# Kernel optimization log

Measured on AMD Instinct MI355X. Metric: run time of the kernel, lower is better.

The kernel has to match this reference:

```python
import jax, jax.numpy as jnp
import numpy as np

N = 8192      # nodes
E = 16384     # edges
G = 512       # graphs
IN = 235      # node feature dim (input_dim)
H = 64        # hidden_dim
ED = 52       # edge feature dim


def setup_inputs() -> dict:
    key = jax.random.key(0)
    ks = jax.random.split(key, 24)
    s = lambda fan_in: 1.0 / np.sqrt(fan_in)
    inp = {}
    inp["x"] = jax.random.normal(ks[0], (N, IN), dtype=jnp.float32)
    inp["edge_index"] = jax.random.randint(ks[1], (2, E), 0, N)
    inp["edge_attr"] = jax.random.uniform(ks[2], (E, ED), dtype=jnp.float32)
    inp["batch"] = jnp.sort(jax.random.randint(ks[3], (N,), 0, G))
    # EdgeModel (nn of nnconv1): Linear(52,128) -> Linear(128, 235*64)
    inp["W1"] = jax.random.normal(ks[4], (128, ED), dtype=jnp.float32) * s(ED)
    inp["b1"] = jnp.zeros((128,), jnp.float32)
    inp["W2"] = jax.random.normal(ks[5], (IN * H, 128), dtype=jnp.float32) * s(128)
    inp["b2"] = jnp.zeros((IN * H,), jnp.float32)
    # NNConv root weight and bias
    inp["root"] = jax.random.normal(ks[6], (IN, H), dtype=jnp.float32) * s(IN)
    inp["conv_b"] = jnp.zeros((H,), jnp.float32)
    # MLP head
    inp["fw1"] = jax.random.normal(ks[7], (128, H), dtype=jnp.float32) * s(H)
    inp["fb1"] = jnp.zeros((128,), jnp.float32)
    inp["fw2"] = jax.random.normal(ks[8], (256, 128), dtype=jnp.float32) * s(128)
    inp["fb2"] = jnp.zeros((256,), jnp.float32)
    inp["fw3"] = jax.random.normal(ks[9], (128, 256), dtype=jnp.float32) * s(256)
    inp["fb3"] = jnp.zeros((128,), jnp.float32)
    inp["fw4"] = jax.random.normal(ks[10], (1, 128), dtype=jnp.float32) * s(128)
    inp["fb4"] = jnp.zeros((1,), jnp.float32)
    return inp


def reference(x, edge_index, edge_attr, batch, W1, b1, W2, b2, root, conv_b,
              fw1, fb1, fw2, fb2, fw3, fb3, fw4, fb4):
    src, dst = edge_index[0], edge_index[1]
    # edge MLP -> per-edge weight matrices [E, IN, H]
    h = edge_attr @ W1.T + b1
    w = (h @ W2.T + b2).reshape(E, IN, H)
    # gather source node feats, per-edge matmul, scatter-add to destinations
    msg = jnp.einsum('ei,eih->eh', x[src], w)          # [E, H]
    agg = jax.ops.segment_sum(msg, dst, num_segments=N)  # [N, H]
    out = jax.nn.relu(agg + x @ root + conv_b)           # NNConv + ReLU
    # global mean pool per graph
    summ = jax.ops.segment_sum(out, batch, num_segments=G)
    cnt = jax.ops.segment_sum(jnp.ones((N, 1), out.dtype), batch, num_segments=G)
    pooled = summ / jnp.maximum(cnt, 1.0)                # [G, H]
    # dense MLP head
    y = jax.nn.relu(pooled @ fw1.T + fb1)
    y = jax.nn.relu(y @ fw2.T + fb2)
    y = jax.nn.relu(y @ fw3.T + fb3)
    return y @ fw4.T + fb4                               # [G, 1]
```

## Files before the change

### kernel.cpp

```cpp
#include <hip/hip_runtime.h>
#include <hip/hip_bf16.h>
#include <stdint.h>

#define N_NODES 8192
#define N_EDGES 16384
#define N_GRAPHS 512
#define IN_DIM 235
#define H_DIM 64
#define ED_DIM 52
#define HID1 128
#define KP 256
#define NB 3328
#define NBP 3584


#define BT_BLOCKS 940
#define EXT_BLOCKS 128
#define ZERO_BLOCKS 16
#define A_BLOCKS 1024
#define PREP_GRID (BT_BLOCKS + EXT_BLOCKS + ZERO_BLOCKS + A_BLOCKS)

#define GEMM_GRID 1728

typedef __bf16 bf16x8 __attribute__((ext_vector_type(8)));
typedef float f32x4 __attribute__((ext_vector_type(4)));

static __device__ inline unsigned short f2bf(float f) {
    union { float f; unsigned u; } v; v.f = f;
    unsigned r = v.u + 0x7FFFu + ((v.u >> 16) & 1u);
    return (unsigned short)(r >> 16);
}

__global__ __launch_bounds__(256) void k_prep(const float* __restrict__ x,
                                              const float* __restrict__ W1,
                                              const float* __restrict__ W2,
                                              const float* __restrict__ b1,
                                              const float* __restrict__ b2,
                                              const float* __restrict__ root,
                                              unsigned short* __restrict__ A,
                                              unsigned short* __restrict__ Bt) {
    __shared__ float w1s[ED_DIM * 132];
    __shared__ float w2s[16 * 132];
    const int bx = blockIdx.x;
    const int t = threadIdx.x;

    if (bx < BT_BLOCKS) {
        const int i = bx >> 2;
        const int by = bx & 3;
        for (int j = t; j < ED_DIM * HID1; j += 256) {
            const int k = j / ED_DIM, d = j - k * ED_DIM;
            w1s[d * 132 + k] = W1[j];
        }
        const float* w2src = W2 + ((size_t)i * 64 + by * 16) * HID1;
        for (int j = t; j < 16 * HID1; j += 256) w2s[(j >> 7) * 132 + (j & 127)] = w2src[j];
        __syncthreads();
        const int hh = t & 15, dq = t >> 4;
        const int h = by * 16 + hh;
        const float4* w2v = (const float4*)&w2s[hh * 132];
        #pragma unroll
        for (int m = 0; m < 4; ++m) {
            const int d = dq + m * 16;
            if (d >= ED_DIM) break;
            const float4* w1v = (const float4*)&w1s[d * 132];
            float acc = 0.f;
            #pragma unroll
            for (int k4 = 0; k4 < HID1 / 4; ++k4) {
                const float4 a = w1v[k4], b = w2v[k4];
                acc += a.x * b.x + a.y * b.y + a.z * b.z + a.w * b.w;
            }
            const int p = ((d >> 2) << 8) + h * 4 + (d & 3);
            Bt[(size_t)p * KP + i] = f2bf(acc);
        }
    } else if (bx < BT_BLOCKS + EXT_BLOCKS) {
        const int j = bx - BT_BLOCKS;
        const int i = t;
        if (i < IN_DIM) {
            float v;
            if (j < 64) {
                v = root[i * H_DIM + j];
            } else {
                const int jj = i * H_DIM + (j - 64);
                float acc = b2[jj];
                const float4* w = (const float4*)(W2 + (size_t)jj * HID1);
                const float4* bv = (const float4*)b1;
                #pragma unroll
                for (int k4 = 0; k4 < HID1 / 4; ++k4) {
                    const float4 a = w[k4], b = bv[k4];
                    acc += a.x * b.x; acc += a.y * b.y; acc += a.z * b.z; acc += a.w * b.w;
                }
                v = acc;
            }
            Bt[(size_t)(NB + j) * KP + i] = f2bf(v);
        }
    } else if (bx < BT_BLOCKS + EXT_BLOCKS + ZERO_BLOCKS) {
        const int z = bx - BT_BLOCKS - EXT_BLOCKS;
        const int TOT = 3456 * 21;
        for (int idx = z * 256 + t; idx < TOT; idx += ZERO_BLOCKS * 256) {
            const int r = idx / 21, c = IN_DIM + idx - r * 21;
            Bt[(size_t)r * KP + c] = 0;
        }
    } else {
        const int j8 = (bx - BT_BLOCKS - EXT_BLOCKS - ZERO_BLOCKS) * 256 + t;
        const int n = j8 >> 5, i0 = (j8 & 31) * 8;
        const float* xr = x + (size_t)n * IN_DIM;
        union { unsigned short us[8]; uint4 q; } pk;
        #pragma unroll
        for (int k = 0; k < 8; ++k) {
            const int i = i0 + k;
            pk.us[k] = (i < IN_DIM) ? f2bf(xr[i]) : (unsigned short)0;
        }
        *(uint4*)(&A[(size_t)j8 * 8]) = pk.q;
    }
}

__global__ __launch_bounds__(256) void k_gemm(const unsigned short* __restrict__ A,
                                              const unsigned short* __restrict__ Bt,
                                              unsigned short* __restrict__ P,
                                              float* __restrict__ agg,
                                              float* __restrict__ xb2,
                                              const float* __restrict__ conv_b) {
    __shared__ unsigned short As[2 * 128 * 32];
    __shared__ unsigned short Bs[2 * 128 * 32];
    const int t = threadIdx.x;
    const int lin = blockIdx.x;
    const int xcd = lin & 7, bi = lin >> 3;
    const int mt = (bi / 27) * 8 + xcd;
    const int nt = bi % 27;
    const int m0 = mt * 128, n0 = nt * 128;
    const int wid = t >> 6, lane = t & 63;
    const int wm = wid & 1;
    const int wn = wid >> 1;
    const int q = lane >> 4, r16 = lane & 15;

    f32x4 acc[4][4] = {};

    auto stage = [&](int k0, int buf) {
        #pragma unroll
        for (int s = 0; s < 2; ++s) {
            const int idx = s * 256 + t;
            const int row = idx >> 2;
            const int lgrp = ((idx & 3) ^ ((row >> 1) & 3)) * 8;
            const unsigned short* ga = &A[(size_t)(m0 + row) * KP + k0 + lgrp];
            const unsigned short* gb = &Bt[(size_t)(n0 + row) * KP + k0 + lgrp];
            char* la = (char*)As + buf * 8192 + s * 4096 + wid * 1024;
            char* lb = (char*)Bs + buf * 8192 + s * 4096 + wid * 1024;
            __builtin_amdgcn_global_load_lds(
                (const __attribute__((address_space(1))) unsigned int*)ga,
                (__attribute__((address_space(3))) unsigned int*)la, 16, 0, 0);
            __builtin_amdgcn_global_load_lds(
                (const __attribute__((address_space(1))) unsigned int*)gb,
                (__attribute__((address_space(3))) unsigned int*)lb, 16, 0, 0);
        }
    };

    stage(0, 0);
    const int pcq = (q ^ ((r16 >> 1) & 3)) * 8;
    #pragma unroll
    for (int it = 0; it < 8; ++it) {
        __syncthreads();
        if (it < 7) stage((it + 1) * 32, (it + 1) & 1);
        const int bo = (it & 1) * 4096;
        bf16x8 af[4], bfr[4];
        #pragma unroll
        for (int mi = 0; mi < 4; ++mi)
            af[mi] = *(const bf16x8*)(&As[bo + (wm * 64 + mi * 16 + r16) * 32 + pcq]);
        #pragma unroll
        for (int ni = 0; ni < 4; ++ni)
            bfr[ni] = *(const bf16x8*)(&Bs[bo + (wn * 64 + ni * 16 + r16) * 32 + pcq]);
        #pragma unroll
        for (int mi = 0; mi < 4; ++mi)
            #pragma unroll
            for (int ni = 0; ni < 4; ++ni)
                acc[mi][ni] = __builtin_amdgcn_mfma_f32_16x16x32_bf16(
                    bfr[ni], af[mi], acc[mi][ni], 0, 0, 0);
    }

    if (nt < 26) {
        #pragma unroll
        for (int mi = 0; mi < 4; ++mi)
            #pragma unroll
            for (int ni = 0; ni < 4; ++ni) {
                const int row = m0 + wm * 64 + mi * 16 + r16;
                const int col = n0 + wn * 64 + ni * 16 + q * 4;
                union { unsigned short us[4]; uint2 u2; } pk;
                #pragma unroll
                for (int rr = 0; rr < 4; ++rr) pk.us[rr] = f2bf(acc[mi][ni][rr]);
                *(uint2*)(&P[(size_t)row * NB + col]) = pk.u2;
            }
    } else {
        #pragma unroll
        for (int mi = 0; mi < 4; ++mi)
            #pragma unroll
            for (int ni = 0; ni < 4; ++ni) {
                const int row = m0 + wm * 64 + mi * 16 + r16;
                const int cl = ni * 16 + q * 4;
                if (wn == 0) {
                    const float4 cb = *(const float4*)&conv_b[cl];
                    float4 v;
                    v.x = acc[mi][ni][0] + cb.x; v.y = acc[mi][ni][1] + cb.y;
                    v.z = acc[mi][ni][2] + cb.z; v.w = acc[mi][ni][3] + cb.w;
                    *(float4*)(&agg[row * H_DIM + cl]) = v;
                } else {
                    float4 v;
                    v.x = acc[mi][ni][0]; v.y = acc[mi][ni][1];
                    v.z = acc[mi][ni][2]; v.w = acc[mi][ni][3];
                    *(float4*)(&xb2[row * H_DIM + cl]) = v;
                }
            }
    }
}

__global__ __launch_bounds__(256) void k_edge(const int* __restrict__ ei,
                                              const float* __restrict__ ea,
                                              const unsigned short* __restrict__ P,
                                              const float* __restrict__ xb2,
                                              float* __restrict__ agg) {
    const int e = (blockIdx.x * 256 + threadIdx.x) >> 6;
    const int h = threadIdx.x & 63;
    if (e >= N_EDGES) return;
    const int s = ei[e], dst = ei[N_EDGES + e];
    const uint2* Pr = (const uint2*)(P + (size_t)s * NB);
    const float4* ev = (const float4*)(ea + (size_t)e * ED_DIM);

    uint2 pv[13];
    #pragma unroll
    for (int j = 0; j < 13; ++j) pv[j] = Pr[j * 64 + h];
    float4 eav[13];
    #pragma unroll
    for (int j = 0; j < 13; ++j) eav[j] = ev[j];

    float acc = xb2[s * H_DIM + h];
    #pragma unroll
    for (int j = 0; j < 13; ++j) {
        union { unsigned u; float f; } a0, a1, b0, b1;
        a0.u = pv[j].x << 16; a1.u = pv[j].x & 0xffff0000u;
        b0.u = pv[j].y << 16; b1.u = pv[j].y & 0xffff0000u;
        acc += eav[j].x * a0.f + eav[j].y * a1.f
             + eav[j].z * b0.f + eav[j].w * b1.f;
    }
    atomicAdd(&agg[dst * H_DIM + h], acc);
}

__global__ __launch_bounds__(256) void k_tail(const float* __restrict__ agg,
                                              const int* __restrict__ batch,
                                              const float* __restrict__ fw1, const float* __restrict__ fb1,
                                              const float* __restrict__ fw2, const float* __restrict__ fb2,
                                              const float* __restrict__ fw3, const float* __restrict__ fb3,
                                              const float* __restrict__ fw4, const float* __restrict__ fb4,
                                              float* __restrict__ out) {
    __shared__ __align__(16) float red[256];
    __shared__ __align__(16) float sp[64];
    __shared__ __align__(16) float s1[128];
    __shared__ __align__(16) float s2[256];
    __shared__ __align__(16) float s3[128];
    const int g = blockIdx.x, t = threadIdx.x;

    int lo = 0, hi = N_NODES;
    while (lo < hi) { const int mid = (lo + hi) >> 1; if (batch[mid] < g) lo = mid + 1; else hi = mid; }
    const int start = lo;
    hi = N_NODES;
    while (lo < hi) { const int mid = (lo + hi) >> 1; if (batch[mid] <= g) lo = mid + 1; else hi = mid; }
    const int end = lo;
    const float inv = 1.0f / fmaxf((float)(end - start), 1.0f);

    float a = 0.f;
    for (int n = start + (t >> 6); n < end; n += 4)
        a += fmaxf(agg[n * H_DIM + (t & 63)], 0.f);
    red[t] = a;
    __syncthreads();
    if (t < 64) sp[t] = (red[t] + red[t + 64] + red[t + 128] + red[t + 192]) * inv;
    __syncthreads();

    if (t < 128) {
        float acc = fb1[t];
        const float4* w = (const float4*)(fw1 + t * 64);
        const float4* sv = (const float4*)sp;
        #pragma unroll
        for (int k = 0; k < 16; ++k) {
            const float4 a4 = w[k], b4 = sv[k];
            acc += a4.x * b4.x; acc += a4.y * b4.y; acc += a4.z * b4.z; acc += a4.w * b4.w;
        }
        s1[t] = fmaxf(acc, 0.f);
    }
    __syncthreads();
    {
        float acc = fb2[t];
        const float4* w = (const float4*)(fw2 + t * 128);
        const float4* sv = (const float4*)s1;
        #pragma unroll
        for (int k = 0; k < 32; ++k) {
            const float4 a4 = w[k], b4 = sv[k];
            acc += a4.x * b4.x; acc += a4.y * b4.y; acc += a4.z * b4.z; acc += a4.w * b4.w;
        }
        s2[t] = fmaxf(acc, 0.f);
    }
    __syncthreads();
    if (t < 128) {
        float acc = fb3[t];
        const float4* w = (const float4*)(fw3 + t * 256);
        const float4* sv = (const float4*)s2;
        #pragma unroll
        for (int k = 0; k < 64; ++k) {
            const float4 a4 = w[k], b4 = sv[k];
            acc += a4.x * b4.x; acc += a4.y * b4.y; acc += a4.z * b4.z; acc += a4.w * b4.w;
        }
        s3[t] = fmaxf(acc, 0.f);
    }
    __syncthreads();
    if (t < 64) {
        float p = s3[t] * fw4[t] + s3[t + 64] * fw4[t + 64];
        #pragma unroll
        for (int off = 32; off > 0; off >>= 1) p += __shfl_down(p, off);
        if (t == 0) out[g] = p + fb4[0];
    }
}

extern "C" void kernel_launch(void* const* d_in, const int* in_sizes, int n_in,
                              void* d_out, int out_size, void* d_ws, size_t ws_size,
                              hipStream_t stream) {
    const float* x      = (const float*)d_in[0];
    const int*   ei     = (const int*)d_in[1];
    const float* ea     = (const float*)d_in[2];
    const int*   batch  = (const int*)d_in[3];
    const float* W1     = (const float*)d_in[4];
    const float* b1     = (const float*)d_in[5];
    const float* W2     = (const float*)d_in[6];
    const float* b2     = (const float*)d_in[7];
    const float* root   = (const float*)d_in[8];
    const float* conv_b = (const float*)d_in[9];
    const float* fw1 = (const float*)d_in[10]; const float* fb1 = (const float*)d_in[11];
    const float* fw2 = (const float*)d_in[12]; const float* fb2 = (const float*)d_in[13];
    const float* fw3 = (const float*)d_in[14]; const float* fb3 = (const float*)d_in[15];
    const float* fw4 = (const float*)d_in[16]; const float* fb4 = (const float*)d_in[17];
    float* out = (float*)d_out;

    char* ws = (char*)d_ws;
    unsigned short* A   = (unsigned short*)(ws);
    unsigned short* Bt  = (unsigned short*)(ws + 4194304);
    unsigned short* P   = (unsigned short*)(ws + 6029312);
    float* agg  = (float*)(ws + 60555264);
    float* xb2  = (float*)(ws + 62652416);

    k_prep<<<dim3(PREP_GRID), dim3(256), 0, stream>>>(x, W1, W2, b1, b2, root, A, Bt);
    k_gemm<<<dim3(GEMM_GRID), dim3(256), 0, stream>>>(A, Bt, P, agg, xb2, conv_b);
    k_edge<<<dim3(N_EDGES / 4), dim3(256), 0, stream>>>(ei, ea, P, xb2, agg);
    k_tail<<<dim3(N_GRAPHS), dim3(256), 0, stream>>>(agg, batch, fw1, fb1, fw2, fb2, fw3, fb3, fw4, fb4, out);
}
```

Baseline: 185.9 us.

## Fuse four kernels into one persistent kernel with grid-wide barriers

Replaces the separate prep, GEMM, edge and tail launches with one persistent kernel of 576 blocks. The blocks loop over the former block indices and are separated by atomic-counter grid barriers. The aim is to remove per-launch overhead and the tail gaps between kernels. In exchange it adds barrier spin cost, needs a memset before each launch, and depends on all 576 blocks being co-resident (launch_bounds 256,3), or the barrier deadlocks or times out. The lower occupancy in the GEMM and edge phases may also hurt throughput.

```diff
diff --git a/kernel.cpp b/kernel.cpp
--- a/kernel.cpp
+++ b/kernel.cpp
@@ -11,16 +11,16 @@
 #define HID1 128
 #define KP 256
 #define NB 3328
-#define NBP 3584
 
 
 #define BT_BLOCKS 940
 #define EXT_BLOCKS 128
 #define ZERO_BLOCKS 16
 #define A_BLOCKS 1024
-#define PREP_GRID (BT_BLOCKS + EXT_BLOCKS + ZERO_BLOCKS + A_BLOCKS)
-
-#define GEMM_GRID 1728
+#define PREP_JOBS (BT_BLOCKS + EXT_BLOCKS + ZERO_BLOCKS + A_BLOCKS)
+
+#define GEMM_JOBS 1728
+#define GRID 576
 
 typedef __bf16 bf16x8 __attribute__((ext_vector_type(8)));
 typedef float f32x4 __attribute__((ext_vector_type(4)));
@@ -31,318 +31,336 @@
     return (unsigned short)(r >> 16);
 }
 
-__global__ __launch_bounds__(256) void k_prep(const float* __restrict__ x,
-                                              const float* __restrict__ W1,
-                                              const float* __restrict__ W2,
-                                              const float* __restrict__ b1,
-                                              const float* __restrict__ b2,
-                                              const float* __restrict__ root,
-                                              unsigned short* __restrict__ A,
-                                              unsigned short* __restrict__ Bt) {
-    __shared__ float w1s[ED_DIM * 132];
-    __shared__ float w2s[16 * 132];
-    const int bx = blockIdx.x;
+struct MegaArgs {
+    const float* x; const int* ei; const float* ea; const int* batch;
+    const float* W1; const float* b1; const float* W2; const float* b2;
+    const float* root; const float* conv_b;
+    const float* fw1; const float* fb1; const float* fw2; const float* fb2;
+    const float* fw3; const float* fb3; const float* fw4; const float* fb4;
+    float* out;
+    unsigned short* A; unsigned short* Bt; unsigned short* P;
+    float* agg; float* xb2;
+    unsigned* bar;
+};
+
+static __device__ inline void grid_barrier(unsigned* ctr, unsigned nb) {
+    __syncthreads();
+    if (threadIdx.x == 0) {
+        __threadfence();
+        atomicAdd(ctr, 1u);
+        unsigned spins = 0;
+        while (atomicAdd(ctr, 0u) < nb) {
+            __builtin_amdgcn_s_sleep(8);
+            if (++spins > 4000000u) break;
+        }
+        __threadfence();
+    }
+    __syncthreads();
+}
+
+__global__ __launch_bounds__(256, 3) void k_mega(MegaArgs a) {
+    __shared__ __align__(16) char smem[35904];
+    const int bid = blockIdx.x;
     const int t = threadIdx.x;
 
-    if (bx < BT_BLOCKS) {
-        const int i = bx >> 2;
-        const int by = bx & 3;
-        for (int j = t; j < ED_DIM * HID1; j += 256) {
-            const int k = j / ED_DIM, d = j - k * ED_DIM;
-            w1s[d * 132 + k] = W1[j];
-        }
-        const float* w2src = W2 + ((size_t)i * 64 + by * 16) * HID1;
-        for (int j = t; j < 16 * HID1; j += 256) w2s[(j >> 7) * 132 + (j & 127)] = w2src[j];
-        __syncthreads();
-        const int hh = t & 15, dq = t >> 4;
-        const int h = by * 16 + hh;
-        const float4* w2v = (const float4*)&w2s[hh * 132];
+    {
+        float* w1s = (float*)smem;
+        float* w2s = (float*)(smem + ED_DIM * 132 * 4);
+        for (int job = bid; job < PREP_JOBS; job += GRID) {
+            if (job < BT_BLOCKS) {
+                const int i = job >> 2;
+                const int by = job & 3;
+                __syncthreads();
+                for (int j = t; j < ED_DIM * HID1; j += 256) {
+                    const int k = j / ED_DIM, d = j - k * ED_DIM;
+                    w1s[d * 132 + k] = a.W1[j];
+                }
+                const float* w2src = a.W2 + ((size_t)i * 64 + by * 16) * HID1;
+                for (int j = t; j < 16 * HID1; j += 256)
+                    w2s[(j >> 7) * 132 + (j & 127)] = w2src[j];
+                __syncthreads();
+                const int hh = t & 15, dq = t >> 4;
+                const int h = by * 16 + hh;
+                const float4* w2v = (const float4*)&w2s[hh * 132];
+                #pragma unroll
+                for (int m = 0; m < 4; ++m) {
+                    const int d = dq + m * 16;
+                    if (d >= ED_DIM) break;
+                    const float4* w1v = (const float4*)&w1s[d * 132];
+                    float acc = 0.f;
+                    #pragma unroll
+                    for (int k4 = 0; k4 < HID1 / 4; ++k4) {
+                        const float4 u = w1v[k4], v = w2v[k4];
+                        acc += u.x * v.x + u.y * v.y + u.z * v.z + u.w * v.w;
+                    }
+                    const int p = ((d >> 2) << 8) + h * 4 + (d & 3);
+                    a.Bt[(size_t)p * KP + i] = f2bf(acc);
+                }
+            } else if (job < BT_BLOCKS + EXT_BLOCKS) {
+                const int j = job - BT_BLOCKS;
+                const int i = t;
+                if (i < IN_DIM) {
+                    float v;
+                    if (j < 64) {
+                        v = a.root[i * H_DIM + j];
+                    } else {
+                        const int jj = i * H_DIM + (j - 64);
+                        float acc = a.b2[jj];
+                        const float4* w = (const float4*)(a.W2 + (size_t)jj * HID1);
+                        const float4* bv = (const float4*)a.b1;
+                        #pragma unroll
+                        for (int k4 = 0; k4 < HID1 / 4; ++k4) {
+                            const float4 u = w[k4], b4 = bv[k4];
+                            acc += u.x * b4.x; acc += u.y * b4.y;
+                            acc += u.z * b4.z; acc += u.w * b4.w;
+                        }
+                        v = acc;
+                    }
+                    a.Bt[(size_t)(NB + j) * KP + i] = f2bf(v);
+                }
+            } else if (job < BT_BLOCKS + EXT_BLOCKS + ZERO_BLOCKS) {
+                const int z = job - BT_BLOCKS - EXT_BLOCKS;
+                const int TOT = 3456 * 21;
+                for (int idx = z * 256 + t; idx < TOT; idx += ZERO_BLOCKS * 256) {
+                    const int r = idx / 21, c = IN_DIM + idx - r * 21;
+                    a.Bt[(size_t)r * KP + c] = 0;
+                }
+            } else {
+                const int j8 = (job - BT_BLOCKS - EXT_BLOCKS - ZERO_BLOCKS) * 256 + t;
+                const int n = j8 >> 5, i0 = (j8 & 31) * 8;
+                const float* xr = a.x + (size_t)n * IN_DIM;
+                union { unsigned short us[8]; uint4 qv; } pk;
+                #pragma unroll
+                for (int k = 0; k < 8; ++k) {
+                    const int i = i0 + k;
+                    pk.us[k] = (i < IN_DIM) ? f2bf(xr[i]) : (unsigned short)0;
+                }
+                *(uint4*)(&a.A[(size_t)j8 * 8]) = pk.qv;
+            }
+        }
+    }
+    grid_barrier(&a.bar[0], GRID);
+
+    {
+        unsigned short* As = (unsigned short*)smem;
+        unsigned short* Bs = As + 8192;
+        const int wid = t >> 6, lane = t & 63;
+        const int wm = wid & 1;
+        const int wn = wid >> 1;
+        const int q = lane >> 4, r16 = lane & 15;
+        const int pcq = (q ^ ((r16 >> 1) & 3)) * 8;
+
+        for (int job = bid; job < GEMM_JOBS; job += GRID) {
+            const int xcd = job & 7, bi = job >> 3;
+            const int mt = (bi / 27) * 8 + xcd;
+            const int nt = bi % 27;
+            const int m0 = mt * 128, n0 = nt * 128;
+
+            f32x4 acc[4][4] = {};
+
+            auto stage = [&](int k0, int buf) {
+                #pragma unroll
+                for (int s2i = 0; s2i < 2; ++s2i) {
+                    const int idx = s2i * 256 + t;
+                    const int row = idx >> 2;
+                    const int lgrp = ((idx & 3) ^ ((row >> 1) & 3)) * 8;
+                    const unsigned short* ga = &a.A[(size_t)(m0 + row) * KP + k0 + lgrp];
+                    const unsigned short* gb = &a.Bt[(size_t)(n0 + row) * KP + k0 + lgrp];
+                    char* la = (char*)As + buf * 8192 + s2i * 4096 + wid * 1024;
+                    char* lb = (char*)Bs + buf * 8192 + s2i * 4096 + wid * 1024;
+                    __builtin_amdgcn_global_load_lds(
+                        (const __attribute__((address_space(1))) unsigned int*)ga,
+                        (__attribute__((address_space(3))) unsigned int*)la, 16, 0, 0);
+                    __builtin_amdgcn_global_load_lds(
+                        (const __attribute__((address_space(1))) unsigned int*)gb,
+                        (__attribute__((address_space(3))) unsigned int*)lb, 16, 0, 0);
+                }
+            };
+
+            stage(0, 0);
+            #pragma unroll
+            for (int it = 0; it < 8; ++it) {
+                __syncthreads();
+                if (it < 7) stage((it + 1) * 32, (it + 1) & 1);
+                const int bo = (it & 1) * 4096;
+                bf16x8 af[4], bfr[4];
+                #pragma unroll
+                for (int mi = 0; mi < 4; ++mi)
+                    af[mi] = *(const bf16x8*)(&As[bo + (wm * 64 + mi * 16 + r16) * 32 + pcq]);
+                #pragma unroll
+                for (int ni = 0; ni < 4; ++ni)
+                    bfr[ni] = *(const bf16x8*)(&Bs[bo + (wn * 64 + ni * 16 + r16) * 32 + pcq]);
+                #pragma unroll
+                for (int mi = 0; mi < 4; ++mi)
+                    #pragma unroll
+                    for (int ni = 0; ni < 4; ++ni)
+                        acc[mi][ni] = __builtin_amdgcn_mfma_f32_16x16x32_bf16(
+                            bfr[ni], af[mi], acc[mi][ni], 0, 0, 0);
+            }
+
+            if (nt < 26) {
+                #pragma unroll
+                for (int mi = 0; mi < 4; ++mi)
+                    #pragma unroll
+                    for (int ni = 0; ni < 4; ++ni) {
+                        const int row = m0 + wm * 64 + mi * 16 + r16;
+                        const int col = n0 + wn * 64 + ni * 16 + q * 4;
+                        union { unsigned short us[4]; uint2 u2; } pk;
+                        #pragma unroll
+                        for (int rr = 0; rr < 4; ++rr) pk.us[rr] = f2bf(acc[mi][ni][rr]);
+                        *(uint2*)(&a.P[(size_t)row * NB + col]) = pk.u2;
+                    }
+            } else {
+                #pragma unroll
+                for (int mi = 0; mi < 4; ++mi)
+                    #pragma unroll
+                    for (int ni = 0; ni < 4; ++ni) {
+                        const int row = m0 + wm * 64 + mi * 16 + r16;
+                        const int cl = ni * 16 + q * 4;
+                        if (wn == 0) {
+                            const float4 cb = *(const float4*)&a.conv_b[cl];
+                            float4 v;
+                            v.x = acc[mi][ni][0] + cb.x; v.y = acc[mi][ni][1] + cb.y;
+                            v.z = acc[mi][ni][2] + cb.z; v.w = acc[mi][ni][3] + cb.w;
+                            *(float4*)(&a.agg[row * H_DIM + cl]) = v;
+                        } else {
+                            float4 v;
+                            v.x = acc[mi][ni][0]; v.y = acc[mi][ni][1];
+                            v.z = acc[mi][ni][2]; v.w = acc[mi][ni][3];
+                            *(float4*)(&a.xb2[row * H_DIM + cl]) = v;
+                        }
+                    }
+            }
+        }
+    }
+    grid_barrier(&a.bar[32], GRID);
+
+    for (int eb = bid; eb < N_EDGES / 4; eb += GRID) {
+        const int e = eb * 4 + (t >> 6);
+        const int h = t & 63;
+        const int s = a.ei[e], dst = a.ei[N_EDGES + e];
+        const uint2* Pr = (const uint2*)(a.P + (size_t)s * NB);
+        const float4* ev = (const float4*)(a.ea + (size_t)e * ED_DIM);
+
+        uint2 pv[13];
         #pragma unroll
-        for (int m = 0; m < 4; ++m) {
-            const int d = dq + m * 16;
-            if (d >= ED_DIM) break;
-            const float4* w1v = (const float4*)&w1s[d * 132];
-            float acc = 0.f;
-            #pragma unroll
-            for (int k4 = 0; k4 < HID1 / 4; ++k4) {
-                const float4 a = w1v[k4], b = w2v[k4];
-                acc += a.x * b.x + a.y * b.y + a.z * b.z + a.w * b.w;
-            }
-            const int p = ((d >> 2) << 8) + h * 4 + (d & 3);
-            Bt[(size_t)p * KP + i] = f2bf(acc);
-        }
-    } else if (bx < BT_BLOCKS + EXT_BLOCKS) {
-        const int j = bx - BT_BLOCKS;
-        const int i = t;
-        if (i < IN_DIM) {
-            float v;
-            if (j < 64) {
-                v = root[i * H_DIM + j];
-            } else {
-                const int jj = i * H_DIM + (j - 64);
-                float acc = b2[jj];
-                const float4* w = (const float4*)(W2 + (size_t)jj * HID1);
-                const float4* bv = (const float4*)b1;
-                #pragma unroll
-                for (int k4 = 0; k4 < HID1 / 4; ++k4) {
-                    const float4 a = w[k4], b = bv[k4];
-                    acc += a.x * b.x; acc += a.y * b.y; acc += a.z * b.z; acc += a.w * b.w;
-                }
-                v = acc;
-            }
-            Bt[(size_t)(NB + j) * KP + i] = f2bf(v);
-        }
-    } else if (bx < BT_BLOCKS + EXT_BLOCKS + ZERO_BLOCKS) {
-        const int z = bx - BT_BLOCKS - EXT_BLOCKS;
-        const int TOT = 3456 * 21;
-        for (int idx = z * 256 + t; idx < TOT; idx += ZERO_BLOCKS * 256) {
-            const int r = idx / 21, c = IN_DIM + idx - r * 21;
-            Bt[(size_t)r * KP + c] = 0;
-        }
-    } else {
-        const int j8 = (bx - BT_BLOCKS - EXT_BLOCKS - ZERO_BLOCKS) * 256 + t;
-        const int n = j8 >> 5, i0 = (j8 & 31) * 8;
-        const float* xr = x + (size_t)n * IN_DIM;
-        union { unsigned short us[8]; uint4 q; } pk;
+        for (int j = 0; j < 13; ++j) pv[j] = Pr[j * 64 + h];
+        float4 eav[13];
         #pragma unroll
-        for (int k = 0; k < 8; ++k) {
-            const int i = i0 + k;
-            pk.us[k] = (i < IN_DIM) ? f2bf(xr[i]) : (unsigned short)0;
-        }
-        *(uint4*)(&A[(size_t)j8 * 8]) = pk.q;
-    }
-}
-
-__global__ __launch_bounds__(256) void k_gemm(const unsigned short* __restrict__ A,
-                                              const unsigned short* __restrict__ Bt,
-                                              unsigned short* __restrict__ P,
-                                              float* __restrict__ agg,
-                                              float* __restrict__ xb2,
-                                              const float* __restrict__ conv_b) {
-    __shared__ unsigned short As[2 * 128 * 32];
-    __shared__ unsigned short Bs[2 * 128 * 32];
-    const int t = threadIdx.x;
-    const int lin = blockIdx.x;
-    const int xcd = lin & 7, bi = lin >> 3;
-    const int mt = (bi / 27) * 8 + xcd;
-    const int nt = bi % 27;
-    const int m0 = mt * 128, n0 = nt * 128;
-    const int wid = t >> 6, lane = t & 63;
-    const int wm = wid & 1;
-    const int wn = wid >> 1;
-    const int q = lane >> 4, r16 = lane & 15;
-
-    f32x4 acc[4][4] = {};
-
-    auto stage = [&](int k0, int buf) {
+        for (int j = 0; j < 13; ++j) eav[j] = ev[j];
+
+        float acc = a.xb2[s * H_DIM + h];
         #pragma unroll
-        for (int s = 0; s < 2; ++s) {
-            const int idx = s * 256 + t;
-            const int row = idx >> 2;
-            const int lgrp = ((idx & 3) ^ ((row >> 1) & 3)) * 8;
-            const unsigned short* ga = &A[(size_t)(m0 + row) * KP + k0 + lgrp];
-            const unsigned short* gb = &Bt[(size_t)(n0 + row) * KP + k0 + lgrp];
-            char* la = (char*)As + buf * 8192 + s * 4096 + wid * 1024;
-            char* lb = (char*)Bs + buf * 8192 + s * 4096 + wid * 1024;
-            __builtin_amdgcn_global_load_lds(
-                (const __attribute__((address_space(1))) unsigned int*)ga,
-                (__attribute__((address_space(3))) unsigned int*)la, 16, 0, 0);
-            __builtin_amdgcn_global_load_lds(
-                (const __attribute__((address_space(1))) unsigned int*)gb,
-                (__attribute__((address_space(3))) unsigned int*)lb, 16, 0, 0);
-        }
-    };
-
-    stage(0, 0);
-    const int pcq = (q ^ ((r16 >> 1) & 3)) * 8;
-    #pragma unroll
-    for (int it = 0; it < 8; ++it) {
-        __syncthreads();
-        if (it < 7) stage((it + 1) * 32, (it + 1) & 1);
-        const int bo = (it & 1) * 4096;
-        bf16x8 af[4], bfr[4];
-        #pragma unroll
-        for (int mi = 0; mi < 4; ++mi)
-            af[mi] = *(const bf16x8*)(&As[bo + (wm * 64 + mi * 16 + r16) * 32 + pcq]);
-        #pragma unroll
-        for (int ni = 0; ni < 4; ++ni)
-            bfr[ni] = *(const bf16x8*)(&Bs[bo + (wn * 64 + ni * 16 + r16) * 32 + pcq]);
-        #pragma unroll
-        for (int mi = 0; mi < 4; ++mi)
-            #pragma unroll
-            for (int ni = 0; ni < 4; ++ni)
-                acc[mi][ni] = __builtin_amdgcn_mfma_f32_16x16x32_bf16(
-                    bfr[ni], af[mi], acc[mi][ni], 0, 0, 0);
-    }
-
-    if (nt < 26) {
-        #pragma unroll
-        for (int mi = 0; mi < 4; ++mi)
-            #pragma unroll
-            for (int ni = 0; ni < 4; ++ni) {
-                const int row = m0 + wm * 64 + mi * 16 + r16;
-                const int col = n0 + wn * 64 + ni * 16 + q * 4;
-                union { unsigned short us[4]; uint2 u2; } pk;
-                #pragma unroll
-                for (int rr = 0; rr < 4; ++rr) pk.us[rr] = f2bf(acc[mi][ni][rr]);
-                *(uint2*)(&P[(size_t)row * NB + col]) = pk.u2;
-            }
-    } else {
-        #pragma unroll
-        for (int mi = 0; mi < 4; ++mi)
-            #pragma unroll
-            for (int ni = 0; ni < 4; ++ni) {
-                const int row = m0 + wm * 64 + mi * 16 + r16;
-                const int cl = ni * 16 + q * 4;
-                if (wn == 0) {
-                    const float4 cb = *(const float4*)&conv_b[cl];
-                    float4 v;
-                    v.x = acc[mi][ni][0] + cb.x; v.y = acc[mi][ni][1] + cb.y;
-                    v.z = acc[mi][ni][2] + cb.z; v.w = acc[mi][ni][3] + cb.w;
-                    *(float4*)(&agg[row * H_DIM + cl]) = v;
-                } else {
-                    float4 v;
-                    v.x = acc[mi][ni][0]; v.y = acc[mi][ni][1];
-                    v.z = acc[mi][ni][2]; v.w = acc[mi][ni][3];
-                    *(float4*)(&xb2[row * H_DIM + cl]) = v;
-                }
-            }
-    }
-}
-
-__global__ __launch_bounds__(256) void k_edge(const int* __restrict__ ei,
-                                              const float* __restrict__ ea,
-                                              const unsigned short* __restrict__ P,
-                                              const float* __restrict__ xb2,
-                                              float* __restrict__ agg) {
-    const int e = (blockIdx.x * 256 + threadIdx.x) >> 6;
-    const int h = threadIdx.x & 63;
-    if (e >= N_EDGES) return;
-    const int s = ei[e], dst = ei[N_EDGES + e];
-    const uint2* Pr = (const uint2*)(P + (size_t)s * NB);
-    const float4* ev = (const float4*)(ea + (size_t)e * ED_DIM);
-
-    uint2 pv[13];
-    #pragma unroll
-    for (int j = 0; j < 13; ++j) pv[j] = Pr[j * 64 + h];
-    float4 eav[13];
-    #pragma unroll
-    for (int j = 0; j < 13; ++j) eav[j] = ev[j];
-
-    float acc = xb2[s * H_DIM + h];
-    #pragma unroll
-    for (int j = 0; j < 13; ++j) {
-        union { unsigned u; float f; } a0, a1, b0, b1;
-        a0.u = pv[j].x << 16; a1.u = pv[j].x & 0xffff0000u;
-        b0.u = pv[j].y << 16; b1.u = pv[j].y & 0xffff0000u;
-        acc += eav[j].x * a0.f + eav[j].y * a1.f
-             + eav[j].z * b0.f + eav[j].w * b1.f;
-    }
-    atomicAdd(&agg[dst * H_DIM + h], acc);
-}
-
-__global__ __launch_bounds__(256) void k_tail(const float* __restrict__ agg,
-                                              const int* __restrict__ batch,
-                                              const float* __restrict__ fw1, const float* __restrict__ fb1,
-                                              const float* __restrict__ fw2, const float* __restrict__ fb2,
-                                              const float* __restrict__ fw3, const float* __restrict__ fb3,
-                                              const float* __restrict__ fw4, const float* __restrict__ fb4,
-                                              float* __restrict__ out) {
-    __shared__ __align__(16) float red[256];
-    __shared__ __align__(16) float sp[64];
-    __shared__ __align__(16) float s1[128];
-    __shared__ __align__(16) float s2[256];
-    __shared__ __align__(16) float s3[128];
-    const int g = blockIdx.x, t = threadIdx.x;
-
-    int lo = 0, hi = N_NODES;
-    while (lo < hi) { const int mid = (lo + hi) >> 1; if (batch[mid] < g) lo = mid + 1; else hi = mid; }
-    const int start = lo;
-    hi = N_NODES;
-    while (lo < hi) { const int mid = (lo + hi) >> 1; if (batch[mid] <= g) lo = mid + 1; else hi = mid; }
-    const int end = lo;
-    const float inv = 1.0f / fmaxf((float)(end - start), 1.0f);
-
-    float a = 0.f;
-    for (int n = start + (t >> 6); n < end; n += 4)
-        a += fmaxf(agg[n * H_DIM + (t & 63)], 0.f);
-    red[t] = a;
-    __syncthreads();
-    if (t < 64) sp[t] = (red[t] + red[t + 64] + red[t + 128] + red[t + 192]) * inv;
-    __syncthreads();
-
-    if (t < 128) {
-        float acc = fb1[t];
-        const float4* w = (const float4*)(fw1 + t * 64);
-        const float4* sv = (const float4*)sp;
-        #pragma unroll
-        for (int k = 0; k < 16; ++k) {
-            const float4 a4 = w[k], b4 = sv[k];
-            acc += a4.x * b4.x; acc += a4.y * b4.y; acc += a4.z * b4.z; acc += a4.w * b4.w;
-        }
-        s1[t] = fmaxf(acc, 0.f);
-    }
-    __syncthreads();
-    {
-        float acc = fb2[t];
-        const float4* w = (const float4*)(fw2 + t * 128);
-        const float4* sv = (const float4*)s1;
-        #pragma unroll
-        for (int k = 0; k < 32; ++k) {
-            const float4 a4 = w[k], b4 = sv[k];
-            acc += a4.x * b4.x; acc += a4.y * b4.y; acc += a4.z * b4.z; acc += a4.w * b4.w;
-        }
-        s2[t] = fmaxf(acc, 0.f);
-    }
-    __syncthreads();
-    if (t < 128) {
-        float acc = fb3[t];
-        const float4* w = (const float4*)(fw3 + t * 256);
-        const float4* sv = (const float4*)s2;
-        #pragma unroll
-        for (int k = 0; k < 64; ++k) {
-            const float4 a4 = w[k], b4 = sv[k];
-            acc += a4.x * b4.x; acc += a4.y * b4.y; acc += a4.z * b4.z; acc += a4.w * b4.w;
-        }
-        s3[t] = fmaxf(acc, 0.f);
-    }
-    __syncthreads();
-    if (t < 64) {
-        float p = s3[t] * fw4[t] + s3[t + 64] * fw4[t + 64];
-        #pragma unroll
-        for (int off = 32; off > 0; off >>= 1) p += __shfl_down(p, off);
-        if (t == 0) out[g] = p + fb4[0];
+        for (int j = 0; j < 13; ++j) {
+            union { unsigned u; float f; } a0, a1, b0, b1;
+            a0.u = pv[j].x << 16; a1.u = pv[j].x & 0xffff0000u;
+            b0.u = pv[j].y << 16; b1.u = pv[j].y & 0xffff0000u;
+            acc += eav[j].x * a0.f + eav[j].y * a1.f
+                 + eav[j].z * b0.f + eav[j].w * b1.f;
+        }
+        atomicAdd(&a.agg[dst * H_DIM + h], acc);
+    }
+    grid_barrier(&a.bar[64], GRID);
+
+    for (int gid = bid; gid < N_GRAPHS; gid += GRID) {
+        float* red = (float*)smem;
+        float* sp  = red + 256;
+        float* s1  = sp + 64;
+        float* s2  = s1 + 128;
+        float* s3  = s2 + 256;
+
+        int lo = 0, hi = N_NODES;
+        while (lo < hi) { const int mid = (lo + hi) >> 1; if (a.batch[mid] < gid) lo = mid + 1; else hi = mid; }
+        const int start = lo;
+        hi = N_NODES;
+        while (lo < hi) { const int mid = (lo + hi) >> 1; if (a.batch[mid] <= gid) lo = mid + 1; else hi = mid; }
+        const int end = lo;
+        const float inv = 1.0f / fmaxf((float)(end - start), 1.0f);
+
+        float acc0 = 0.f;
+        for (int n = start + (t >> 6); n < end; n += 4)
+            acc0 += fmaxf(a.agg[n * H_DIM + (t & 63)], 0.f);
+        red[t] = acc0;
+        __syncthreads();
+        if (t < 64) sp[t] = (red[t] + red[t + 64] + red[t + 128] + red[t + 192]) * inv;
+        __syncthreads();
+
+        if (t < 128) {
+            float acc = a.fb1[t];
+            const float4* w = (const float4*)(a.fw1 + t * 64);
+            const float4* sv = (const float4*)sp;
+            #pragma unroll
+            for (int k = 0; k < 16; ++k) {
+                const float4 u = w[k], b4 = sv[k];
+                acc += u.x * b4.x; acc += u.y * b4.y; acc += u.z * b4.z; acc += u.w * b4.w;
+            }
+            s1[t] = fmaxf(acc, 0.f);
+        }
+        __syncthreads();
+        {
+            float acc = a.fb2[t];
+            const float4* w = (const float4*)(a.fw2 + t * 128);
+            const float4* sv = (const float4*)s1;
+            #pragma unroll
+            for (int k = 0; k < 32; ++k) {
+                const float4 u = w[k], b4 = sv[k];
+                acc += u.x * b4.x; acc += u.y * b4.y; acc += u.z * b4.z; acc += u.w * b4.w;
+            }
+            s2[t] = fmaxf(acc, 0.f);
+        }
+        __syncthreads();
+        if (t < 128) {
+            float acc = a.fb3[t];
+            const float4* w = (const float4*)(a.fw3 + t * 256);
+            const float4* sv = (const float4*)s2;
+            #pragma unroll
+            for (int k = 0; k < 64; ++k) {
+                const float4 u = w[k], b4 = sv[k];
+                acc += u.x * b4.x; acc += u.y * b4.y; acc += u.z * b4.z; acc += u.w * b4.w;
+            }
+            s3[t] = fmaxf(acc, 0.f);
+        }
+        __syncthreads();
+        if (t < 64) {
+            float p = s3[t] * a.fw4[t] + s3[t + 64] * a.fw4[t + 64];
+            #pragma unroll
+            for (int off = 32; off > 0; off >>= 1) p += __shfl_down(p, off);
+            if (t == 0) a.out[gid] = p + a.fb4[0];
+        }
+        __syncthreads();
     }
 }
 
 extern "C" void kernel_launch(void* const* d_in, const int* in_sizes, int n_in,
                               void* d_out, int out_size, void* d_ws, size_t ws_size,
                               hipStream_t stream) {
-    const float* x      = (const float*)d_in[0];
-    const int*   ei     = (const int*)d_in[1];
-    const float* ea     = (const float*)d_in[2];
-    const int*   batch  = (const int*)d_in[3];
-    const float* W1     = (const float*)d_in[4];
-    const float* b1     = (const float*)d_in[5];
-    const float* W2     = (const float*)d_in[6];
-    const float* b2     = (const float*)d_in[7];
-    const float* root   = (const float*)d_in[8];
-    const float* conv_b = (const float*)d_in[9];
-    const float* fw1 = (const float*)d_in[10]; const float* fb1 = (const float*)d_in[11];
-    const float* fw2 = (const float*)d_in[12]; const float* fb2 = (const float*)d_in[13];
-    const float* fw3 = (const float*)d_in[14]; const float* fb3 = (const float*)d_in[15];
-    const float* fw4 = (const float*)d_in[16]; const float* fb4 = (const float*)d_in[17];
-    float* out = (float*)d_out;
-
     char* ws = (char*)d_ws;
     unsigned short* A   = (unsigned short*)(ws);
     unsigned short* Bt  = (unsigned short*)(ws + 4194304);
     unsigned short* P   = (unsigned short*)(ws + 6029312);
     float* agg  = (float*)(ws + 60555264);
     float* xb2  = (float*)(ws + 62652416);
-
-    k_prep<<<dim3(PREP_GRID), dim3(256), 0, stream>>>(x, W1, W2, b1, b2, root, A, Bt);
-    k_gemm<<<dim3(GEMM_GRID), dim3(256), 0, stream>>>(A, Bt, P, agg, xb2, conv_b);
-    k_edge<<<dim3(N_EDGES / 4), dim3(256), 0, stream>>>(ei, ea, P, xb2, agg);
-    k_tail<<<dim3(N_GRAPHS), dim3(256), 0, stream>>>(agg, batch, fw1, fb1, fw2, fb2, fw3, fb3, fw4, fb4, out);
+    unsigned* bar = (unsigned*)(ws + 64749568);
+
+    MegaArgs ma;
+    ma.x      = (const float*)d_in[0];
+    ma.ei     = (const int*)d_in[1];
+    ma.ea     = (const float*)d_in[2];
+    ma.batch  = (const int*)d_in[3];
+    ma.W1     = (const float*)d_in[4];
+    ma.b1     = (const float*)d_in[5];
+    ma.W2     = (const float*)d_in[6];
+    ma.b2     = (const float*)d_in[7];
+    ma.root   = (const float*)d_in[8];
+    ma.conv_b = (const float*)d_in[9];
+    ma.fw1 = (const float*)d_in[10]; ma.fb1 = (const float*)d_in[11];
+    ma.fw2 = (const float*)d_in[12]; ma.fb2 = (const float*)d_in[13];
+    ma.fw3 = (const float*)d_in[14]; ma.fb3 = (const float*)d_in[15];
+    ma.fw4 = (const float*)d_in[16]; ma.fb4 = (const float*)d_in[17];
+    ma.out = (float*)d_out;
+    ma.A = A; ma.Bt = Bt; ma.P = P; ma.agg = agg; ma.xb2 = xb2;
+    ma.bar = bar;
+
+    hipMemsetAsync(bar, 0, 384, stream);
+    k_mega<<<dim3(GRID), dim3(256), 0, stream>>>(ma);
 }
```

New measurement: 414.9 us. +123.2%, slower.
